# Performance work log

Measured on AMD Instinct MI355X. Metric: run time of the kernel, lower is better.

Reference implementation:

```python
import jax, jax.numpy as jnp
import numpy as np

L, D, H, K, M = 4, 512, 8, 10, 2048  # depth, dim, heads, relation bins, mlp_dim
DH = D // H
B, N = 4, 512
EPS = 1e-5


def setup_inputs() -> dict:
    key = jax.random.key(0)
    ks = jax.random.split(key, 12)
    s = lambda i, shape, scale: jax.random.normal(ks[i], shape, jnp.float32) * scale
    return {
        "x": s(0, (B, N, D), 1.0),
        "coord": jax.random.uniform(ks[1], (B, N, 2), dtype=jnp.float32) * 20.0,  # spread over ~K distance bins
        "ln1_g": jnp.ones((L, D)), "ln1_b": jnp.zeros((L, D)),
        "wq": s(2, (L, D, D), 0.02), "bq": jnp.zeros((L, D)),
        "wk": s(3, (L, D, D), 0.02), "bk": jnp.zeros((L, D)),
        "wv": s(4, (L, D, D), 0.02), "bv": jnp.zeros((L, D)),
        "wo": s(5, (L, D, D), 0.02), "bo": jnp.zeros((L, D)),
        "rel_k": s(6, (L, K, DH), 0.02), "rel_v": s(7, (L, K, DH), 0.02),
        "ln2_g": jnp.ones((L, D)), "ln2_b": jnp.zeros((L, D)),
        "w1": s(8, (L, D, M), 0.02), "b1": jnp.zeros((L, M)),
        "w2": s(9, (L, M, D), 0.02), "b2": jnp.zeros((L, D)),
        "lnf_g": jnp.ones((D,)), "lnf_b": jnp.zeros((D,)),
    }


def _ln(x, g, b):
    m = jnp.mean(x, -1, keepdims=True)
    v = jnp.mean((x - m) ** 2, -1, keepdims=True)
    return (x - m) * jax.lax.rsqrt(v + EPS) * g + b


def _forward(x, coord, ln1_g, ln1_b, wq, bq, wk, bk, wv, bv, wo, bo,
             rel_k, rel_v, ln2_g, ln2_b, w1, b1, w2, b2, lnf_g, lnf_b):
    b_, n_, _ = x.shape
    # pairwise Euclidean distances bucketized + clipped to K relation bins
    dist = jnp.linalg.norm(coord[:, :, None, :] - coord[:, None, :, :], axis=-1)  # [B,N,N]
    idx = jnp.clip(jnp.floor(dist), 0, K - 1).astype(jnp.int32)                   # [B,N,N]
    scale = DH ** -0.5
    for l in range(L):
        h = _ln(x, ln1_g[l], ln1_b[l])
        q = (h @ wq[l] + bq[l]).reshape(b_, n_, H, DH).transpose(0, 2, 1, 3)  # [B,H,N,DH]
        k = (h @ wk[l] + bk[l]).reshape(b_, n_, H, DH).transpose(0, 2, 1, 3)
        v = (h @ wv[l] + bv[l]).reshape(b_, n_, H, DH).transpose(0, 2, 1, 3)
        aK = rel_k[l][idx]  # [B,N,N,DH] relation key embeddings
        aV = rel_v[l][idx]  # [B,N,N,DH] relation value embeddings
        scores = (jnp.einsum('bhnd,bhmd->bhnm', q, k)
                  + jnp.einsum('bhnd,bnmd->bhnm', q, aK)) * scale
        attn = jax.nn.softmax(scores, axis=-1)  # [B,H,N,N]
        o = (jnp.einsum('bhnm,bhmd->bhnd', attn, v)
             + jnp.einsum('bhnm,bnmd->bhnd', attn, aV))
        o = o.transpose(0, 2, 1, 3).reshape(b_, n_, D) @ wo[l] + bo[l]
        x = o + x  # residual around attention
        h2 = _ln(x, ln2_g[l], ln2_b[l])
        x = jax.nn.gelu(h2 @ w1[l] + b1[l], approximate=False) @ w2[l] + b2[l] + x  # FFN residual
    return _ln(x, lnf_g, lnf_b)


def reference(x, coord, ln1_g, ln1_b, wq, bq, wk, bk, wv, bv, wo, bo,
              rel_k, rel_v, ln2_g, ln2_b, w1, b1, w2, b2, lnf_g, lnf_b):
    return _forward(x, coord, ln1_g, ln1_b, wq, bq, wk, bk, wv, bv, wo, bo,
                    rel_k, rel_v, ln2_g, ln2_b, w1, b1, w2, b2, lnf_g, lnf_b)
```

## Files before the change

### kernel.cpp

```cpp
#include <hip/hip_runtime.h>
#include <cmath>

constexpr int Bx = 4, Nx = 512, Dx = 512, Hx = 8, DHx = 64, Kx = 10, Mx = 2048, Lx = 4;
constexpr float EPSx = 1e-5f;
typedef unsigned short u16;
typedef __attribute__((ext_vector_type(8))) short short8;
typedef __attribute__((ext_vector_type(4))) float f32x4;

__device__ __forceinline__ u16 f2bf(float f) {
  unsigned u = __builtin_bit_cast(unsigned, f);
  return (u16)((u + 0x7fffu + ((u >> 16) & 1u)) >> 16);
}
__device__ __forceinline__ float bf2f(u16 h) {
  unsigned u = ((unsigned)h) << 16;
  return __builtin_bit_cast(float, u);
}
__device__ __forceinline__ void gload16(const void* g, void* l) {
  __builtin_amdgcn_global_load_lds((const __attribute__((address_space(1))) void*)g,
                                   (__attribute__((address_space(3))) void*)l, 16, 0, 0);
}
__device__ __forceinline__ float wave_max(float v) {
  #pragma unroll
  for (int off = 1; off < 64; off <<= 1) v = fmaxf(v, __shfl_xor(v, off));
  return v;
}
__device__ __forceinline__ float wave_sum(float v) {
  #pragma unroll
  for (int off = 1; off < 64; off <<= 1) v += __shfl_xor(v, off);
  return v;
}

__global__ __launch_bounds__(256) void idx_kernel(const float* __restrict__ coord,
                                                  unsigned char* __restrict__ idx8) {
  int t = blockIdx.x * 256 + threadIdx.x;
  int m = t % Nx;
  int n = (t / Nx) % Nx;
  int b = t / (Nx * Nx);
  float dx = coord[(b * Nx + n) * 2 + 0] - coord[(b * Nx + m) * 2 + 0];
  float dy = coord[(b * Nx + n) * 2 + 1] - coord[(b * Nx + m) * 2 + 1];
  float dist = sqrtf(dx * dx + dy * dy);
  int bin = (int)floorf(dist);
  bin = bin < 0 ? 0 : (bin > Kx - 1 ? Kx - 1 : bin);
  idx8[t] = (unsigned char)bin;
}

__global__ __launch_bounds__(256) void wsplitT_kernel(const float* __restrict__ W,
                                                      u16* __restrict__ Thi,
                                                      u16* __restrict__ Tlo,
                                                      int K, int N, size_t dst_lstride) {
  __shared__ float tile[32][33];
  int l = blockIdx.z;
  const float* Wl = W + (size_t)l * K * N;
  u16* hi = Thi + (size_t)l * dst_lstride;
  u16* lo = Tlo + (size_t)l * dst_lstride;
  int n0 = blockIdx.x * 32, k0 = blockIdx.y * 32;
  int tx = threadIdx.x & 31, ty = threadIdx.x >> 5;
  #pragma unroll
  for (int i = 0; i < 4; i++) {
    int kk = ty + i * 8;
    tile[kk][tx] = Wl[(size_t)(k0 + kk) * N + n0 + tx];
  }
  __syncthreads();
  #pragma unroll
  for (int i = 0; i < 4; i++) {
    int nn = ty + i * 8;
    float v = tile[tx][nn];
    u16 h = f2bf(v);
    hi[(size_t)(n0 + nn) * K + k0 + tx] = h;
    lo[(size_t)(n0 + nn) * K + k0 + tx] = f2bf(v - bf2f(h));
  }
}

__global__ __launch_bounds__(256) void ln_kernel(const float* __restrict__ x,
                                                 const float* __restrict__ g,
                                                 const float* __restrict__ bta,
                                                 float* __restrict__ out) {
  __shared__ float red[256];
  int row = blockIdx.x;
  int tid = threadIdx.x;
  const float2 v = reinterpret_cast<const float2*>(x + (size_t)row * Dx)[tid];

  red[tid] = v.x + v.y;
  __syncthreads();
  for (int s = 128; s > 0; s >>= 1) { if (tid < s) red[tid] += red[tid + s]; __syncthreads(); }
  float mean = red[0] * (1.0f / Dx);
  __syncthreads();

  float d0 = v.x - mean, d1 = v.y - mean;
  red[tid] = d0 * d0 + d1 * d1;
  __syncthreads();
  for (int s = 128; s > 0; s >>= 1) { if (tid < s) red[tid] += red[tid + s]; __syncthreads(); }
  float rstd = rsqrtf(red[0] * (1.0f / Dx) + EPSx);
  __syncthreads();

  float2 gg = reinterpret_cast<const float2*>(g)[tid];
  float2 bb = reinterpret_cast<const float2*>(bta)[tid];
  float2 o;
  o.x = d0 * rstd * gg.x + bb.x;
  o.y = d1 * rstd * gg.y + bb.y;
  reinterpret_cast<float2*>(out + (size_t)row * Dx)[tid] = o;
}

__global__ __launch_bounds__(256) void ln_split_kernel(const float* __restrict__ x,
                                                       const float* __restrict__ g,
                                                       const float* __restrict__ bta,
                                                       u16* __restrict__ hhi,
                                                       u16* __restrict__ hlo) {
  __shared__ float red[256];
  int row = blockIdx.x;
  int tid = threadIdx.x;
  const float2 v = reinterpret_cast<const float2*>(x + (size_t)row * Dx)[tid];

  red[tid] = v.x + v.y;
  __syncthreads();
  for (int s = 128; s > 0; s >>= 1) { if (tid < s) red[tid] += red[tid + s]; __syncthreads(); }
  float mean = red[0] * (1.0f / Dx);
  __syncthreads();

  float d0 = v.x - mean, d1 = v.y - mean;
  red[tid] = d0 * d0 + d1 * d1;
  __syncthreads();
  for (int s = 128; s > 0; s >>= 1) { if (tid < s) red[tid] += red[tid + s]; __syncthreads(); }
  float rstd = rsqrtf(red[0] * (1.0f / Dx) + EPSx);
  __syncthreads();

  float2 gg = reinterpret_cast<const float2*>(g)[tid];
  float2 bb = reinterpret_cast<const float2*>(bta)[tid];
  float ox = d0 * rstd * gg.x + bb.x;
  float oy = d1 * rstd * gg.y + bb.y;
  u16 hx = f2bf(ox), hy = f2bf(oy);
  ushort2 hv = {hx, hy};
  ushort2 lv = {f2bf(ox - bf2f(hx)), f2bf(oy - bf2f(hy))};
  reinterpret_cast<ushort2*>(hhi + (size_t)row * Dx)[tid] = hv;
  reinterpret_cast<ushort2*>(hlo + (size_t)row * Dx)[tid] = lv;
}

template <int BM, int BN, int EPI>
__global__ __launch_bounds__(256) void gemm_mfma(
    const u16* __restrict__ Ahi, const u16* __restrict__ Alo,
    const u16* __restrict__ Bhi, const u16* __restrict__ Blo,
    const float* __restrict__ bias,
    float* __restrict__ C, u16* __restrict__ Chi, u16* __restrict__ Clo,
    int M, int Nn, int Kk) {
  constexpr int FM = BM / 32, FN = BN / 32;
  __shared__ __align__(16) u16 lds[(BM + BN) * 64];
  u16* lAhi = lds;
  u16* lAlo = lds + BM * 32;
  u16* lBhi = lds + BM * 64;
  u16* lBlo = lds + BM * 64 + BN * 32;

  const int tid = threadIdx.x;
  const int lane = tid & 63;
  const int wid = tid >> 6;
  const int wr = wid >> 1, wc = wid & 1;
  const int row0 = blockIdx.y * BM, col0 = blockIdx.x * BN;
  const int kg = (lane >> 4) * 8;
  const int lr = lane & 15;

  f32x4 acc[FM][FN];
  #pragma unroll
  for (int m = 0; m < FM; m++)
    #pragma unroll
    for (int n = 0; n < FN; n++) acc[m][n] = (f32x4)(0.0f);

  constexpr int AR = (BM * 32) / 2048;
  constexpr int BR = (BN * 32) / 2048;

  for (int kt = 0; kt < Kk; kt += 32) {
    #pragma unroll
    for (int r = 0; r < AR; r++) {
      int e = r * 2048 + tid * 8;
      int row = e >> 5, kc = e & 31;
      size_t go = (size_t)(row0 + row) * Kk + kt + kc;
      gload16(Ahi + go, lAhi + e);
      gload16(Alo + go, lAlo + e);
    }
    #pragma unroll
    for (int r = 0; r < BR; r++) {
      int e = r * 2048 + tid * 8;
      int row = e >> 5, kc = e & 31;
      size_t go = (size_t)(col0 + row) * Kk + kt + kc;
      gload16(Bhi + go, lBhi + e);
      gload16(Blo + go, lBlo + e);
    }
    __syncthreads();

    short8 ah[FM], al[FM], bh[FN], bl[FN];
    #pragma unroll
    for (int m = 0; m < FM; m++) {
      int off = (wr * (BM / 2) + m * 16 + lr) * 32 + kg;
      ah[m] = *reinterpret_cast<const short8*>(lAhi + off);
      al[m] = *reinterpret_cast<const short8*>(lAlo + off);
    }
    #pragma unroll
    for (int n = 0; n < FN; n++) {
      int off = (wc * (BN / 2) + n * 16 + lr) * 32 + kg;
      bh[n] = *reinterpret_cast<const short8*>(lBhi + off);
      bl[n] = *reinterpret_cast<const short8*>(lBlo + off);
    }
    #pragma unroll
    for (int m = 0; m < FM; m++)
      #pragma unroll
      for (int n = 0; n < FN; n++) {
        acc[m][n] = __builtin_amdgcn_mfma_f32_16x16x32_bf16(ah[m], bh[n], acc[m][n], 0, 0, 0);
        acc[m][n] = __builtin_amdgcn_mfma_f32_16x16x32_bf16(ah[m], bl[n], acc[m][n], 0, 0, 0);
        acc[m][n] = __builtin_amdgcn_mfma_f32_16x16x32_bf16(al[m], bh[n], acc[m][n], 0, 0, 0);
      }
    __syncthreads();
  }

  const int rbase = (lane >> 4) * 4;
  #pragma unroll
  for (int m = 0; m < FM; m++) {
    #pragma unroll
    for (int n = 0; n < FN; n++) {
      int cidx = col0 + wc * (BN / 2) + n * 16 + lr;
      float bcol = bias[cidx];
      #pragma unroll
      for (int r = 0; r < 4; r++) {
        int row = row0 + wr * (BM / 2) + m * 16 + rbase + r;
        size_t o = (size_t)row * Nn + cidx;
        float val = acc[m][n][r] + bcol;
        if constexpr (EPI == 1) {
          C[o] = val + C[o];
        } else if constexpr (EPI == 2) {
          val = 0.5f * val * (1.0f + erff(val * 0.70710678118654752f));
          u16 h = f2bf(val);
          Chi[o] = h;
          Clo[o] = f2bf(val - bf2f(h));
        } else {
          u16 h = f2bf(val);
          Chi[o] = h;
          Clo[o] = f2bf(val - bf2f(h));
        }
      }
    }
  }
}

template <int KC>
__global__ __launch_bounds__(256) void gemm_splitk(
    const u16* __restrict__ Ahi, const u16* __restrict__ Alo,
    const u16* __restrict__ Bhi, const u16* __restrict__ Blo,
    const float* __restrict__ bias, float* __restrict__ C,
    int M, int Nn, int Kk) {
  constexpr int BM = 64, BN = 128;
  constexpr int FM = 2, FN = 4;
  __shared__ __align__(16) u16 lds[(BM + BN) * 64];
  u16* lAhi = lds;
  u16* lAlo = lds + BM * 32;
  u16* lBhi = lds + BM * 64;
  u16* lBlo = lds + BM * 64 + BN * 32;

  const int tid = threadIdx.x;
  const int lane = tid & 63;
  const int wid = tid >> 6;
  const int wr = wid >> 1, wc = wid & 1;
  const int row0 = blockIdx.y * BM, col0 = blockIdx.x * BN;
  const int kz = blockIdx.z;
  const int kbase = kz * KC;
  const int kg = (lane >> 4) * 8;
  const int lr = lane & 15;

  f32x4 acc[FM][FN];
  #pragma unroll
  for (int m = 0; m < FM; m++)
    #pragma unroll
    for (int n = 0; n < FN; n++) acc[m][n] = (f32x4)(0.0f);

  for (int kt = kbase; kt < kbase + KC; kt += 32) {
    {
      int e = tid * 8;
      int row = e >> 5, kc = e & 31;
      size_t go = (size_t)(row0 + row) * Kk + kt + kc;
      gload16(Ahi + go, lAhi + e);
      gload16(Alo + go, lAlo + e);
    }
    #pragma unroll
    for (int r = 0; r < 2; r++) {
      int e = r * 2048 + tid * 8;
      int row = e >> 5, kc = e & 31;
      size_t go = (size_t)(col0 + row) * Kk + kt + kc;
      gload16(Bhi + go, lBhi + e);
      gload16(Blo + go, lBlo + e);
    }
    __syncthreads();

    short8 ah[FM], al[FM], bh[FN], bl[FN];
    #pragma unroll
    for (int m = 0; m < FM; m++) {
      int off = (wr * 32 + m * 16 + lr) * 32 + kg;
      ah[m] = *reinterpret_cast<const short8*>(lAhi + off);
      al[m] = *reinterpret_cast<const short8*>(lAlo + off);
    }
    #pragma unroll
    for (int n = 0; n < FN; n++) {
      int off = (wc * 64 + n * 16 + lr) * 32 + kg;
      bh[n] = *reinterpret_cast<const short8*>(lBhi + off);
      bl[n] = *reinterpret_cast<const short8*>(lBlo + off);
    }
    #pragma unroll
    for (int m = 0; m < FM; m++)
      #pragma unroll
      for (int n = 0; n < FN; n++) {
        acc[m][n] = __builtin_amdgcn_mfma_f32_16x16x32_bf16(ah[m], bh[n], acc[m][n], 0, 0, 0);
        acc[m][n] = __builtin_amdgcn_mfma_f32_16x16x32_bf16(ah[m], bl[n], acc[m][n], 0, 0, 0);
        acc[m][n] = __builtin_amdgcn_mfma_f32_16x16x32_bf16(al[m], bh[n], acc[m][n], 0, 0, 0);
      }
    __syncthreads();
  }

  const int rbase = (lane >> 4) * 4;
  #pragma unroll
  for (int m = 0; m < FM; m++) {
    #pragma unroll
    for (int n = 0; n < FN; n++) {
      int cidx = col0 + wc * 64 + n * 16 + lr;
      float bcol = (kz == 0) ? bias[cidx] : 0.0f;
      #pragma unroll
      for (int r = 0; r < 4; r++) {
        int row = row0 + wr * 32 + m * 16 + rbase + r;
        atomicAdd(&C[(size_t)row * Nn + cidx], acc[m][n][r] + bcol);
      }
    }
  }
}

__global__ __launch_bounds__(256) void gemm_qkv(
    const u16* __restrict__ Ahi, const u16* __restrict__ Alo,
    const u16* __restrict__ Bhi, const u16* __restrict__ Blo,
    const float* __restrict__ bq, const float* __restrict__ bk,
    const float* __restrict__ bv,
    u16* __restrict__ qhi, u16* __restrict__ qlo,
    u16* __restrict__ khi, u16* __restrict__ klo,
    u16* __restrict__ vThi, u16* __restrict__ vTlo) {
  constexpr int Kk = 512;
  __shared__ __align__(16) u16 lds[128 * 64];
  u16* lAhi = lds;
  u16* lAlo = lds + 2048;
  u16* lBhi = lds + 4096;
  u16* lBlo = lds + 6144;

  const int tid = threadIdx.x;
  const int lane = tid & 63;
  const int wid = tid >> 6;
  const int wr = wid >> 1, wc = wid & 1;
  const int row0 = blockIdx.y * 64, col0 = blockIdx.x * 64;
  const int kg = (lane >> 4) * 8;
  const int lr = lane & 15;

  f32x4 acc[2][2];
  #pragma unroll
  for (int m = 0; m < 2; m++)
    #pragma unroll
    for (int n = 0; n < 2; n++) acc[m][n] = (f32x4)(0.0f);

  for (int kt = 0; kt < Kk; kt += 32) {
    int e = tid * 8;
    int row = e >> 5, kc = e & 31;
    size_t ga = (size_t)(row0 + row) * Kk + kt + kc;
    size_t gb = (size_t)(col0 + row) * Kk + kt + kc;
    gload16(Ahi + ga, lAhi + e);
    gload16(Alo + ga, lAlo + e);
    gload16(Bhi + gb, lBhi + e);
    gload16(Blo + gb, lBlo + e);
    __syncthreads();

    short8 ah[2], al[2], bh[2], bl[2];
    #pragma unroll
    for (int m = 0; m < 2; m++) {
      int off = (wr * 32 + m * 16 + lr) * 32 + kg;
      ah[m] = *reinterpret_cast<const short8*>(lAhi + off);
      al[m] = *reinterpret_cast<const short8*>(lAlo + off);
    }
    #pragma unroll
    for (int n = 0; n < 2; n++) {
      int off = (wc * 32 + n * 16 + lr) * 32 + kg;
      bh[n] = *reinterpret_cast<const short8*>(lBhi + off);
      bl[n] = *reinterpret_cast<const short8*>(lBlo + off);
    }
    #pragma unroll
    for (int m = 0; m < 2; m++)
      #pragma unroll
      for (int n = 0; n < 2; n++) {
        acc[m][n] = __builtin_amdgcn_mfma_f32_16x16x32_bf16(ah[m], bh[n], acc[m][n], 0, 0, 0);
        acc[m][n] = __builtin_amdgcn_mfma_f32_16x16x32_bf16(ah[m], bl[n], acc[m][n], 0, 0, 0);
        acc[m][n] = __builtin_amdgcn_mfma_f32_16x16x32_bf16(al[m], bh[n], acc[m][n], 0, 0, 0);
      }
    __syncthreads();
  }

  const int rbase = (lane >> 4) * 4;
  #pragma unroll
  for (int m = 0; m < 2; m++) {
    #pragma unroll
    for (int n = 0; n < 2; n++) {
      int cidx = col0 + wc * 32 + n * 16 + lr;
      float bcol = cidx < 512 ? bq[cidx]
                  : (cidx < 1024 ? bk[cidx - 512] : bv[cidx - 1024]);
      #pragma unroll
      for (int r = 0; r < 4; r++) {
        int row = row0 + wr * 32 + m * 16 + rbase + r;
        float val = acc[m][n][r] + bcol;
        u16 h = f2bf(val);
        u16 lo2 = f2bf(val - bf2f(h));
        if (cidx < 512) {
          size_t o = (size_t)row * 512 + cidx;
          qhi[o] = h; qlo[o] = lo2;
        } else if (cidx < 1024) {
          size_t o = (size_t)row * 512 + (cidx - 512);
          khi[o] = h; klo[o] = lo2;
        } else {
          size_t o = (size_t)(cidx - 1024) * 2048 + row;
          vThi[o] = h; vTlo[o] = lo2;
        }
      }
    }
  }
}

__global__ __launch_bounds__(256) void qrel_kernel(const u16* __restrict__ qhi,
                                                   const u16* __restrict__ qlo,
                                                   const float* __restrict__ relk,
                                                   float* __restrict__ qrel) {
  int t = blockIdx.x * 256 + threadIdx.x;
  if (t >= Bx * Nx * Hx * Kx) return;
  int kbin = t % Kx;
  int h = (t / Kx) % Hx;
  int bn = t / (Kx * Hx);
  size_t base = (size_t)bn * Dx + h * DHx;
  const float* rr = relk + kbin * DHx;
  float s = 0.f;
  #pragma unroll
  for (int d = 0; d < DHx; d++)
    s += (bf2f(qhi[base + d]) + bf2f(qlo[base + d])) * rr[d];
  qrel[t] = s;
}

__global__ __launch_bounds__(256) void scores_mfma(
    const u16* __restrict__ qhi, const u16* __restrict__ qlo,
    const u16* __restrict__ khi, const u16* __restrict__ klo,
    const float* __restrict__ qrel, const unsigned char* __restrict__ idx8,
    float* __restrict__ scores) {
  __shared__ __align__(16) u16 lds[4 * 2048];
  u16* lQh = lds;
  u16* lQl = lds + 2048;
  u16* lKh = lds + 4096;
  u16* lKl = lds + 6144;

  const int bh = blockIdx.z;
  const int b = bh >> 3, h = bh & 7;
  const int n0 = blockIdx.y * 64, m0 = blockIdx.x * 64;
  const int tid = threadIdx.x;
  const int lane = tid & 63;
  const int wid = tid >> 6;
  const int wr = wid >> 1, wc = wid & 1;
  const int kg = (lane >> 4) * 8;
  const int lr = lane & 15;

  f32x4 acc[2][2];
  #pragma unroll
  for (int m = 0; m < 2; m++)
    #pragma unroll
    for (int n = 0; n < 2; n++) acc[m][n] = (f32x4)(0.0f);

  for (int kt = 0; kt < DHx; kt += 32) {
    int e = tid * 8;
    int row = e >> 5, kc = e & 31;
    size_t gq = (size_t)(b * Nx + n0 + row) * Dx + h * DHx + kt + kc;
    size_t gk = (size_t)(b * Nx + m0 + row) * Dx + h * DHx + kt + kc;
    gload16(qhi + gq, lQh + e);
    gload16(qlo + gq, lQl + e);
    gload16(khi + gk, lKh + e);
    gload16(klo + gk, lKl + e);
    __syncthreads();

    short8 ah[2], al[2], bhf[2], blf[2];
    #pragma unroll
    for (int m = 0; m < 2; m++) {
      int off = (wr * 32 + m * 16 + lr) * 32 + kg;
      ah[m] = *reinterpret_cast<const short8*>(lQh + off);
      al[m] = *reinterpret_cast<const short8*>(lQl + off);
    }
    #pragma unroll
    for (int n = 0; n < 2; n++) {
      int off = (wc * 32 + n * 16 + lr) * 32 + kg;
      bhf[n] = *reinterpret_cast<const short8*>(lKh + off);
      blf[n] = *reinterpret_cast<const short8*>(lKl + off);
    }
    #pragma unroll
    for (int m = 0; m < 2; m++)
      #pragma unroll
      for (int n = 0; n < 2; n++) {
        acc[m][n] = __builtin_amdgcn_mfma_f32_16x16x32_bf16(ah[m], bhf[n], acc[m][n], 0, 0, 0);
        acc[m][n] = __builtin_amdgcn_mfma_f32_16x16x32_bf16(ah[m], blf[n], acc[m][n], 0, 0, 0);
        acc[m][n] = __builtin_amdgcn_mfma_f32_16x16x32_bf16(al[m], bhf[n], acc[m][n], 0, 0, 0);
      }
    __syncthreads();
  }

  const int rbase = (lane >> 4) * 4;
  #pragma unroll
  for (int m = 0; m < 2; m++) {
    #pragma unroll
    for (int n = 0; n < 2; n++) {
      int mg = m0 + wc * 32 + n * 16 + lr;
      #pragma unroll
      for (int r = 0; r < 4; r++) {
        int ng = n0 + wr * 32 + m * 16 + rbase + r;
        unsigned char iv = idx8[(size_t)(b * Nx + ng) * Nx + mg];
        float bias = qrel[((size_t)(b * Nx + ng) * Hx + h) * Kx + iv];
        scores[((size_t)bh * Nx + ng) * Nx + mg] = (acc[m][n][r] + bias) * 0.125f;
      }
    }
  }
}

__global__ __launch_bounds__(256) void softmax_wave(float* scores,
                                                    const unsigned char* __restrict__ idx8,
                                                    float* __restrict__ attnK) {
  const int tid = threadIdx.x;
  const int lane = tid & 63;
  const int wid = tid >> 6;
  const int row = blockIdx.x * 4 + wid;
  const int n = row & (Nx - 1);
  const int b = row >> 12;
  float* s = scores + (size_t)row * Nx;

  float4 v0 = reinterpret_cast<const float4*>(s)[lane * 2];
  float4 v1 = reinterpret_cast<const float4*>(s)[lane * 2 + 1];
  float p[8] = {v0.x, v0.y, v0.z, v0.w, v1.x, v1.y, v1.z, v1.w};

  float mx = p[0];
  #pragma unroll
  for (int j = 1; j < 8; j++) mx = fmaxf(mx, p[j]);
  mx = wave_max(mx);

  float sum = 0.f;
  #pragma unroll
  for (int j = 0; j < 8; j++) { p[j] = expf(p[j] - mx); sum += p[j]; }
  sum = wave_sum(sum);
  float inv = 1.0f / sum;

  const unsigned char* idr = idx8 + (size_t)(b * Nx + n) * Nx + lane * 8;
  uchar4 c0 = *reinterpret_cast<const uchar4*>(idr);
  uchar4 c1 = *reinterpret_cast<const uchar4*>(idr + 4);
  int iv[8] = {c0.x, c0.y, c0.z, c0.w, c1.x, c1.y, c1.z, c1.w};

  float bins[Kx];
  #pragma unroll
  for (int kk = 0; kk < Kx; kk++) bins[kk] = 0.f;
  #pragma unroll
  for (int j = 0; j < 8; j++)
    #pragma unroll
    for (int kk = 0; kk < Kx; kk++) bins[kk] += (iv[j] == kk) ? p[j] : 0.f;
  #pragma unroll
  for (int kk = 0; kk < Kx; kk++) bins[kk] = wave_sum(bins[kk]);

  short8 sv;
  #pragma unroll
  for (int j = 0; j < 8; j++) sv[j] = (short)f2bf(p[j] * inv);
  u16* prow = reinterpret_cast<u16*>(s);
  *reinterpret_cast<short8*>(prow + lane * 8) = sv;

  if (lane == 0) {
    #pragma unroll
    for (int kk = 0; kk < Kx; kk++) attnK[(size_t)row * Kx + kk] = bins[kk] * inv;
  }
}

__global__ __launch_bounds__(256) void pv_mfma(
    const u16* __restrict__ P,
    const u16* __restrict__ vThi, const u16* __restrict__ vTlo,
    const float* __restrict__ attnK, const float* __restrict__ rel_v,
    u16* __restrict__ ohi, u16* __restrict__ olo) {
  __shared__ __align__(16) u16 lP[2 * 32 * 32];
  __shared__ __align__(16) u16 sVh[2 * 64 * 32];
  __shared__ __align__(16) u16 sVl[2 * 64 * 32];
  __shared__ float aKs[32][Kx];
  __shared__ float RelVs[Kx][DHx];

  const int bh = blockIdx.y;
  const int b = bh >> 3, h = bh & 7;
  const int n0 = blockIdx.x * 32;
  const int tid = threadIdx.x;
  const int lane = tid & 63;
  const int wid = tid >> 6;
  const int wr = wid >> 1, wc = wid & 1;
  const int kg = (lane >> 4) * 8;
  const int lr = lane & 15;
  const int rbase = (lane >> 4) * 4;

  for (int t = tid; t < 32 * Kx; t += 256)
    aKs[t / Kx][t % Kx] = attnK[(size_t)(bh * Nx + n0 + t / Kx) * Kx + t % Kx];
  for (int t = tid; t < Kx * DHx; t += 256)
    RelVs[t / DHx][t % DHx] = rel_v[t];

  f32x4 acc[2];
  acc[0] = (f32x4)(0.0f);
  acc[1] = (f32x4)(0.0f);

  for (int mt = 0; mt < Nx; mt += 64) {
    {
      int e = tid * 8;
      int ks = e >> 10, row = (e >> 5) & 31, col = e & 31;
      gload16(P + (size_t)(bh * Nx + n0 + row) * 1024 + mt + ks * 32 + col, lP + e);
    }
    #pragma unroll
    for (int rr = 0; rr < 2; rr++) {
      int e = rr * 2048 + tid * 8;
      int ks = e >> 11, dh = (e >> 5) & 63, col = e & 31;
      size_t gv = (size_t)(h * DHx + dh) * 2048 + b * Nx + mt + ks * 32 + col;
      gload16(vThi + gv, sVh + e);
      gload16(vTlo + gv, sVl + e);
    }
    __syncthreads();

    short8 pa[2];
    #pragma unroll
    for (int ks = 0; ks < 2; ks++)
      pa[ks] = *reinterpret_cast<const short8*>(lP + ks * 1024 + (wr * 16 + lr) * 32 + kg);
    #pragma unroll
    for (int f = 0; f < 2; f++) {
      int dh = wc * 32 + f * 16 + lr;
      #pragma unroll
      for (int ks = 0; ks < 2; ks++) {
        short8 vh = *reinterpret_cast<const short8*>(sVh + ks * 2048 + dh * 32 + kg);
        short8 vl = *reinterpret_cast<const short8*>(sVl + ks * 2048 + dh * 32 + kg);
        acc[f] = __builtin_amdgcn_mfma_f32_16x16x32_bf16(pa[ks], vh, acc[f], 0, 0, 0);
        acc[f] = __builtin_amdgcn_mfma_f32_16x16x32_bf16(pa[ks], vl, acc[f], 0, 0, 0);
      }
    }
    __syncthreads();
  }

  #pragma unroll
  for (int f = 0; f < 2; f++) {
    int dl = wc * 32 + f * 16 + lr;
    float rv[Kx];
    #pragma unroll
    for (int kk = 0; kk < Kx; kk++) rv[kk] = RelVs[kk][dl];
    #pragma unroll
    for (int r = 0; r < 4; r++) {
      int nl = wr * 16 + rbase + r;
      float val = acc[f][r];
      #pragma unroll
      for (int kk = 0; kk < Kx; kk++) val += aKs[nl][kk] * rv[kk];
      size_t oo = (size_t)(b * Nx + n0 + nl) * Dx + h * DHx + dl;
      u16 hh = f2bf(val);
      ohi[oo] = hh;
      olo[oo] = f2bf(val - bf2f(hh));
    }
  }
}

extern "C" void kernel_launch(void* const* d_in, const int* in_sizes, int n_in,
                              void* d_out, int out_size, void* d_ws, size_t ws_size,
                              hipStream_t stream) {
  const float* x_in  = (const float*)d_in[0];
  const float* coord = (const float*)d_in[1];
  const float* ln1_g = (const float*)d_in[2];
  const float* ln1_b = (const float*)d_in[3];
  const float* wq    = (const float*)d_in[4];
  const float* bq    = (const float*)d_in[5];
  const float* wk    = (const float*)d_in[6];
  const float* bk    = (const float*)d_in[7];
  const float* wv    = (const float*)d_in[8];
  const float* bv    = (const float*)d_in[9];
  const float* wo    = (const float*)d_in[10];
  const float* bo    = (const float*)d_in[11];
  const float* rel_k = (const float*)d_in[12];
  const float* rel_v = (const float*)d_in[13];
  const float* ln2_g = (const float*)d_in[14];
  const float* ln2_b = (const float*)d_in[15];
  const float* w1    = (const float*)d_in[16];
  const float* b1    = (const float*)d_in[17];
  const float* w2    = (const float*)d_in[18];
  const float* b2    = (const float*)d_in[19];
  const float* lnf_g = (const float*)d_in[20];
  const float* lnf_b = (const float*)d_in[21];

  float* x = (float*)d_out;
  constexpr size_t BND  = (size_t)Bx * Nx * Dx;
  constexpr size_t SC   = (size_t)Bx * Hx * Nx * Nx;
  constexpr size_t RELS = (size_t)Bx * Nx * Hx * Kx;
  constexpr size_t QKVW = (size_t)1536 * 512;

  char* w = (char*)d_ws;
  size_t off = 0;
  auto nxt = [&](size_t bytes) -> void* {
    void* p = w + off;
    off = (off + bytes + 255) & ~(size_t)255;
    return p;
  };
  unsigned char* idxb = (unsigned char*)nxt((size_t)Bx * Nx * Nx);
  float* scores = (float*)nxt(4ull * SC);
  float* qrel   = (float*)nxt(4ull * RELS);
  float* attnK  = (float*)nxt(4ull * RELS);
  u16* qhi = (u16*)nxt(2ull * BND);
  u16* qlo = (u16*)nxt(2ull * BND);
  u16* khi = (u16*)nxt(2ull * BND);
  u16* klo = (u16*)nxt(2ull * BND);
  u16* vThi = (u16*)nxt(2ull * BND);
  u16* vTlo = (u16*)nxt(2ull * BND);
  u16* hhi = (u16*)nxt(2ull * BND);
  u16* hlo = (u16*)nxt(2ull * BND);
  u16* ohi = (u16*)nxt(2ull * BND);
  u16* olo = (u16*)nxt(2ull * BND);
  u16* wqkvThi = (u16*)nxt(2ull * Lx * QKVW);
  u16* wqkvTlo = (u16*)nxt(2ull * Lx * QKVW);
  u16* woThi = (u16*)nxt(2ull * Lx * Dx * Dx);
  u16* woTlo = (u16*)nxt(2ull * Lx * Dx * Dx);
  u16* w1Thi = (u16*)nxt(2ull * Lx * Dx * Mx);
  u16* w1Tlo = (u16*)nxt(2ull * Lx * Dx * Mx);
  u16* w2Thi = (u16*)nxt(2ull * Lx * Mx * Dx);
  u16* w2Tlo = (u16*)nxt(2ull * Lx * Mx * Dx);
  u16* f1hi = (u16*)scores;
  u16* f1lo = f1hi + (size_t)(Bx * Nx) * Mx;
  u16* Pbuf = (u16*)scores;

  hipMemcpyAsync(x, x_in, BND * sizeof(float), hipMemcpyDeviceToDevice, stream);
  idx_kernel<<<(Bx * Nx * Nx) / 256, 256, 0, stream>>>(coord, idxb);

  dim3 gw(Dx / 32, Dx / 32, Lx);
  wsplitT_kernel<<<gw, 256, 0, stream>>>(wq, wqkvThi, wqkvTlo, Dx, Dx, QKVW);
  wsplitT_kernel<<<gw, 256, 0, stream>>>(wk, wqkvThi + (size_t)512 * 512,
                                         wqkvTlo + (size_t)512 * 512, Dx, Dx, QKVW);
  wsplitT_kernel<<<gw, 256, 0, stream>>>(wv, wqkvThi + (size_t)1024 * 512,
                                         wqkvTlo + (size_t)1024 * 512, Dx, Dx, QKVW);
  wsplitT_kernel<<<gw, 256, 0, stream>>>(wo, woThi, woTlo, Dx, Dx, (size_t)Dx * Dx);
  wsplitT_kernel<<<dim3(Mx / 32, Dx / 32, Lx), 256, 0, stream>>>(
      w1, w1Thi, w1Tlo, Dx, Mx, (size_t)Dx * Mx);
  wsplitT_kernel<<<dim3(Dx / 32, Mx / 32, Lx), 256, 0, stream>>>(
      w2, w2Thi, w2Tlo, Mx, Dx, (size_t)Mx * Dx);

  const int Mrows = Bx * Nx;
  dim3 gqkv(1536 / 64, Mrows / 64);
  dim3 gw1(Mx / 128, Mrows / 64);
  dim3 gwo(Dx / 128, Mrows / 64, 4);
  dim3 gw2(Dx / 128, Mrows / 64, 4);
  dim3 gs(Nx / 64, Nx / 64, Bx * Hx);
  dim3 gpv(Nx / 32, Bx * Hx);

  for (int l = 0; l < Lx; l++) {
    size_t wD = (size_t)l * Dx * Dx;
    size_t w1o = (size_t)l * Dx * Mx;
    size_t w2o = (size_t)l * Mx * Dx;

    ln_split_kernel<<<Mrows, 256, 0, stream>>>(x, ln1_g + l * Dx, ln1_b + l * Dx, hhi, hlo);
    gemm_qkv<<<gqkv, 256, 0, stream>>>(hhi, hlo,
                                       wqkvThi + (size_t)l * QKVW, wqkvTlo + (size_t)l * QKVW,
                                       bq + l * Dx, bk + l * Dx, bv + l * Dx,
                                       qhi, qlo, khi, klo, vThi, vTlo);
    qrel_kernel<<<(Bx * Nx * Hx * Kx + 255) / 256, 256, 0, stream>>>(
        qhi, qlo, rel_k + (size_t)l * Kx * DHx, qrel);
    scores_mfma<<<gs, 256, 0, stream>>>(qhi, qlo, khi, klo, qrel, idxb, scores);
    softmax_wave<<<Bx * Hx * Nx / 4, 256, 0, stream>>>(scores, idxb, attnK);
    pv_mfma<<<gpv, 256, 0, stream>>>(Pbuf, vThi, vTlo, attnK,
                                     rel_v + (size_t)l * Kx * DHx, ohi, olo);
    gemm_splitk<128><<<gwo, 256, 0, stream>>>(ohi, olo, woThi + wD, woTlo + wD,
                                              bo + l * Dx, x, Mrows, Dx, Dx);
    ln_split_kernel<<<Mrows, 256, 0, stream>>>(x, ln2_g + l * Dx, ln2_b + l * Dx, hhi, hlo);
    gemm_mfma<64, 128, 2><<<gw1, 256, 0, stream>>>(hhi, hlo, w1Thi + w1o, w1Tlo + w1o,
                                                   b1 + l * Mx, nullptr, f1hi, f1lo,
                                                   Mrows, Mx, Dx);
    gemm_splitk<512><<<gw2, 256, 0, stream>>>(f1hi, f1lo, w2Thi + w2o, w2Tlo + w2o,
                                              b2 + l * Dx, x, Mrows, Dx, Mx);
  }
  ln_kernel<<<Mrows, 256, 0, stream>>>(x, lnf_g, lnf_b, x);
}
```

Measured before the change: 789.7 us.

## Double-buffer LDS tiles in GEMM kernels and remap workgroups across XCDs

Converts the three MFMA GEMM kernels (generic, split-K, QKV) to double-buffered LDS staging, issuing the global-to-LDS loads for the next K tile before computing on the current one. This is meant to overlap load latency with the MFMA work. It also remaps the block index so consecutive tiles go to the same XCD (id&7 striding), aiming for better L2 locality. The cost is twice the LDS per block, which can lower occupancy, and the remap assumes the block count is divisible by 8.

After: 790.4 us. No clear change (+0.1%).

```diff
diff --git a/kernel.cpp b/kernel.cpp
--- a/kernel.cpp
+++ b/kernel.cpp
@@ -143,60 +143,77 @@
     float* __restrict__ C, u16* __restrict__ Chi, u16* __restrict__ Clo,
     int M, int Nn, int Kk) {
   constexpr int FM = BM / 32, FN = BN / 32;
-  __shared__ __align__(16) u16 lds[(BM + BN) * 64];
-  u16* lAhi = lds;
-  u16* lAlo = lds + BM * 32;
-  u16* lBhi = lds + BM * 64;
-  u16* lBlo = lds + BM * 64 + BN * 32;
+  constexpr int HALF = (BM + BN) * 64;
+  __shared__ __align__(16) u16 lds[2 * HALF];
 
   const int tid = threadIdx.x;
   const int lane = tid & 63;
   const int wid = tid >> 6;
   const int wr = wid >> 1, wc = wid & 1;
-  const int row0 = blockIdx.y * BM, col0 = blockIdx.x * BN;
+  const int nwg = gridDim.x * gridDim.y;
+  const int id = blockIdx.y * gridDim.x + blockIdx.x;
+  const int nid = (id & 7) * (nwg >> 3) + (id >> 3);
+  const int row0 = (nid % gridDim.y) * BM;
+  const int col0 = (nid / gridDim.y) * BN;
   const int kg = (lane >> 4) * 8;
   const int lr = lane & 15;
 
-  f32x4 acc[FM][FN];
-  #pragma unroll
-  for (int m = 0; m < FM; m++)
-    #pragma unroll
-    for (int n = 0; n < FN; n++) acc[m][n] = (f32x4)(0.0f);
-
   constexpr int AR = (BM * 32) / 2048;
   constexpr int BR = (BN * 32) / 2048;
 
-  for (int kt = 0; kt < Kk; kt += 32) {
+  auto stage = [&](int buf, int kt) {
+    u16* lA  = lds + buf * HALF;
+    u16* lAl = lA + BM * 32;
+    u16* lB  = lA + BM * 64;
+    u16* lBl = lA + BM * 64 + BN * 32;
     #pragma unroll
     for (int r = 0; r < AR; r++) {
       int e = r * 2048 + tid * 8;
       int row = e >> 5, kc = e & 31;
       size_t go = (size_t)(row0 + row) * Kk + kt + kc;
-      gload16(Ahi + go, lAhi + e);
-      gload16(Alo + go, lAlo + e);
+      gload16(Ahi + go, lA + e);
+      gload16(Alo + go, lAl + e);
     }
     #pragma unroll
     for (int r = 0; r < BR; r++) {
       int e = r * 2048 + tid * 8;
       int row = e >> 5, kc = e & 31;
       size_t go = (size_t)(col0 + row) * Kk + kt + kc;
-      gload16(Bhi + go, lBhi + e);
-      gload16(Blo + go, lBlo + e);
-    }
-    __syncthreads();
+      gload16(Bhi + go, lB + e);
+      gload16(Blo + go, lBl + e);
+    }
+  };
+
+  f32x4 acc[FM][FN];
+  #pragma unroll
+  for (int m = 0; m < FM; m++)
+    #pragma unroll
+    for (int n = 0; n < FN; n++) acc[m][n] = (f32x4)(0.0f);
+
+  stage(0, 0);
+  __syncthreads();
+  const int nt = Kk / 32;
+  for (int t = 0; t < nt; ++t) {
+    const int cur = t & 1;
+    if (t + 1 < nt) stage(cur ^ 1, (t + 1) * 32);
+
+    const u16* lA  = lds + cur * HALF;
+    const u16* lAl = lA + BM * 32;
+    const u16* lB  = lA + BM * 64;
+    const u16* lBl = lA + BM * 64 + BN * 32;
 
     short8 ah[FM], al[FM], bh[FN], bl[FN];
     #pragma unroll
     for (int m = 0; m < FM; m++) {
       int off = (wr * (BM / 2) + m * 16 + lr) * 32 + kg;
-      ah[m] = *reinterpret_cast<const short8*>(lAhi + off);
-      al[m] = *reinterpret_cast<const short8*>(lAlo + off);
+      ah[m] = *reinterpret_cast<const short8*>(lA + off);
+      al[m] = *reinterpret_cast<const short8*>(lAl + off);
     }
     #pragma unroll
     for (int n = 0; n < FN; n++) {
       int off = (wc * (BN / 2) + n * 16 + lr) * 32 + kg;
-      bh[n] = *reinterpret_cast<const short8*>(lBhi + off);
-      bl[n] = *reinterpret_cast<const short8*>(lBlo + off);
+      bh[n] = *reinterpret_cast<const short8*>(lB + off);
+      bl[n] = *reinterpret_cast<const short8*>(lBl + off);
     }
     #pragma unroll
     for (int m = 0; m < FM; m++)
@@ -246,58 +263,75 @@
     int M, int Nn, int Kk) {
   constexpr int BM = 64, BN = 128;
   constexpr int FM = 2, FN = 4;
-  __shared__ __align__(16) u16 lds[(BM + BN) * 64];
-  u16* lAhi = lds;
-  u16* lAlo = lds + BM * 32;
-  u16* lBhi = lds + BM * 64;
-  u16* lBlo = lds + BM * 64 + BN * 32;
+  constexpr int HALF = (BM + BN) * 64;
+  __shared__ __align__(16) u16 lds[2 * HALF];
 
   const int tid = threadIdx.x;
   const int lane = tid & 63;
   const int wid = tid >> 6;
   const int wr = wid >> 1, wc = wid & 1;
-  const int row0 = blockIdx.y * BM, col0 = blockIdx.x * BN;
+  const int nwg = gridDim.x * gridDim.y;
+  const int id = blockIdx.y * gridDim.x + blockIdx.x;
+  const int nid = (id & 7) * (nwg >> 3) + (id >> 3);
+  const int row0 = (nid % gridDim.y) * BM;
+  const int col0 = (nid / gridDim.y) * BN;
   const int kz = blockIdx.z;
   const int kbase = kz * KC;
   const int kg = (lane >> 4) * 8;
   const int lr = lane & 15;
 
-  f32x4 acc[FM][FN];
-  #pragma unroll
-  for (int m = 0; m < FM; m++)
-    #pragma unroll
-    for (int n = 0; n < FN; n++) acc[m][n] = (f32x4)(0.0f);
-
-  for (int kt = kbase; kt < kbase + KC; kt += 32) {
+  auto stage = [&](int buf, int kt) {
+    u16* lA  = lds + buf * HALF;
+    u16* lAl = lA + BM * 32;
+    u16* lB  = lA + BM * 64;
+    u16* lBl = lA + BM * 64 + BN * 32;
     {
       int e = tid * 8;
       int row = e >> 5, kc = e & 31;
       size_t go = (size_t)(row0 + row) * Kk + kt + kc;
-      gload16(Ahi + go, lAhi + e);
-      gload16(Alo + go, lAlo + e);
+      gload16(Ahi + go, lA + e);
+      gload16(Alo + go, lAl + e);
     }
     #pragma unroll
     for (int r = 0; r < 2; r++) {
       int e = r * 2048 + tid * 8;
       int row = e >> 5, kc = e & 31;
       size_t go = (size_t)(col0 + row) * Kk + kt + kc;
-      gload16(Bhi + go, lBhi + e);
-      gload16(Blo + go, lBlo + e);
-    }
-    __syncthreads();
+      gload16(Bhi + go, lB + e);
+      gload16(Blo + go, lBl + e);
+    }
+  };
+
+  f32x4 acc[FM][FN];
+  #pragma unroll
+  for (int m = 0; m < FM; m++)
+    #pragma unroll
+    for (int n = 0; n < FN; n++) acc[m][n] = (f32x4)(0.0f);
+
+  stage(0, kbase);
+  __syncthreads();
+  constexpr int nt = KC / 32;
+  for (int t = 0; t < nt; ++t) {
+    const int cur = t & 1;
+    if (t + 1 < nt) stage(cur ^ 1, kbase + (t + 1) * 32);
+
+    const u16* lA  = lds + cur * HALF;
+    const u16* lAl = lA + BM * 32;
+    const u16* lB  = lA + BM * 64;
+    const u16* lBl = lA + BM * 64 + BN * 32;
 
     short8 ah[FM], al[FM], bh[FN], bl[FN];
     #pragma unroll
     for (int m = 0; m < FM; m++) {
       int off = (wr * 32 + m * 16 + lr) * 32 + kg;
-      ah[m] = *reinterpret_cast<const short8*>(lAhi + off);
-      al[m] = *reinterpret_cast<const short8*>(lAlo + off);
+      ah[m] = *reinterpret_cast<const short8*>(lA + off);
+      al[m] = *reinterpret_cast<const short8*>(lAl + off);
     }
     #pragma unroll
     for (int n = 0; n < FN; n++) {
       int off = (wc * 64 + n * 16 + lr) * 32 + kg;
-      bh[n] = *reinterpret_cast<const short8*>(lBhi + off);
-      bl[n] = *reinterpret_cast<const short8*>(lBlo + off);
+      bh[n] = *reinterpret_cast<const short8*>(lB + off);
+      bl[n] = *reinterpret_cast<const short8*>(lBl + off);
     }
     #pragma unroll
     for (int m = 0; m < FM; m++)
@@ -335,49 +369,66 @@
     u16* __restrict__ khi, u16* __restrict__ klo,
     u16* __restrict__ vThi, u16* __restrict__ vTlo) {
   constexpr int Kk = 512;
-  __shared__ __align__(16) u16 lds[128 * 64];
-  u16* lAhi = lds;
-  u16* lAlo = lds + 2048;
-  u16* lBhi = lds + 4096;
-  u16* lBlo = lds + 6144;
+  constexpr int HALF = 128 * 64;
+  __shared__ __align__(16) u16 lds[2 * HALF];
 
   const int tid = threadIdx.x;
   const int lane = tid & 63;
   const int wid = tid >> 6;
   const int wr = wid >> 1, wc = wid & 1;
-  const int row0 = blockIdx.y * 64, col0 = blockIdx.x * 64;
+  const int nwg = gridDim.x * gridDim.y;
+  const int id = blockIdx.y * gridDim.x + blockIdx.x;
+  const int nid = (id & 7) * (nwg >> 3) + (id >> 3);
+  const int row0 = (nid % gridDim.y) * 64;
+  const int col0 = (nid / gridDim.y) * 64;
   const int kg = (lane >> 4) * 8;
   const int lr = lane & 15;
 
-  f32x4 acc[2][2];
-  #pragma unroll
-  for (int m = 0; m < 2; m++)
-    #pragma unroll
-    for (int n = 0; n < 2; n++) acc[m][n] = (f32x4)(0.0f);
-
-  for (int kt = 0; kt < Kk; kt += 32) {
+  auto stage = [&](int buf, int kt) {
+    u16* lA  = lds + buf * HALF;
+    u16* lAl = lA + 2048;
+    u16* lB  = lA + 4096;
+    u16* lBl = lA + 6144;
     int e = tid * 8;
     int row = e >> 5, kc = e & 31;
     size_t ga = (size_t)(row0 + row) * Kk + kt + kc;
     size_t gb = (size_t)(col0 + row) * Kk + kt + kc;
-    gload16(Ahi + ga, lAhi + e);
-    gload16(Alo + ga, lAlo + e);
-    gload16(Bhi + gb, lBhi + e);
-    gload16(Blo + gb, lBlo + e);
-    __syncthreads();
+    gload16(Ahi + ga, lA + e);
+    gload16(Alo + ga, lAl + e);
+    gload16(Bhi + gb, lB + e);
+    gload16(Blo + gb, lBl + e);
+  };
+
+  f32x4 acc[2][2];
+  #pragma unroll
+  for (int m = 0; m < 2; m++)
+    #pragma unroll
+    for (int n = 0; n < 2; n++) acc[m][n] = (f32x4)(0.0f);
+
+  stage(0, 0);
+  __syncthreads();
+  constexpr int nt = Kk / 32;
+  for (int t = 0; t < nt; ++t) {
+    const int cur = t & 1;
+    if (t + 1 < nt) stage(cur ^ 1, (t + 1) * 32);
+
+    const u16* lA  = lds + cur * HALF;
+    const u16* lAl = lA + 2048;
+    const u16* lB  = lA + 4096;
+    const u16* lBl = lA + 6144;
 
     short8 ah[2], al[2], bh[2], bl[2];
     #pragma unroll
     for (int m = 0; m < 2; m++) {
       int off = (wr * 32 + m * 16 + lr) * 32 + kg;
-      ah[m] = *reinterpret_cast<const short8*>(lAhi + off);
-      al[m] = *reinterpret_cast<const short8*>(lAlo + off);
+      ah[m] = *reinterpret_cast<const short8*>(lA + off);
+      al[m] = *reinterpret_cast<const short8*>(lAl + off);
     }
     #pragma unroll
     for (int n = 0; n < 2; n++) {
       int off = (wc * 32 + n * 16 + lr) * 32 + kg;
-      bh[n] = *reinterpret_cast<const short8*>(lBhi + off);
-      bl[n] = *reinterpret_cast<const short8*>(lBlo + off);
+      bh[n] = *reinterpret_cast<const short8*>(lB + off);
+      bl[n] = *reinterpret_cast<const short8*>(lBl + off);
     }
     #pragma unroll
     for (int m = 0; m < 2; m++)
```
